# Kernel optimization log

Measured on AMD Instinct MI355X. Metric: run time of the kernel, lower is better.

## Reference

```python
import jax, jax.numpy as jnp
import numpy as np

B = 256
INPUT_DIM = 78464
PC_DIM = 1936
K = 9          # number of step1 sub-models
C = 600        # features per sub-model


def setup_inputs() -> dict:
    key = jax.random.key(0)
    ks = jax.random.split(key, 8)
    x = jax.random.normal(ks[0], (B, INPUT_DIM + 2), dtype=jnp.float32)
    center = jax.random.normal(ks[1], (INPUT_DIM,), dtype=jnp.float32)
    rotation = jax.random.normal(ks[2], (INPUT_DIM, PC_DIM), dtype=jnp.float32) * 0.01
    feats = jax.random.randint(ks[3], (K, C), 0, PC_DIM + 2, dtype=jnp.int32)
    w1 = jax.random.normal(ks[4], (K, C), dtype=jnp.float32) * 0.05   # stacked Linear(C,1) weights
    b1 = jax.random.normal(ks[5], (K,), dtype=jnp.float32)            # stacked biases
    w2 = jax.random.normal(ks[6], (K + 2,), dtype=jnp.float32) * 0.1  # step2 weight
    b2 = jax.random.normal(ks[7], (1,), dtype=jnp.float32)            # step2 bias
    return dict(x=x, center=center, rotation=rotation, feats=feats,
                w1=w1, b1=b1, w2=w2, b2=b2)


def reference(x, center, rotation, feats, w1, b1, w2, b2):
    age = x[:, -1]      # [B]
    female = x[:, -2]   # [B]
    # PCA projection: center and rotate
    p = (x[:, :-2] - center) @ rotation                    # [B, PC_DIM]
    p = jnp.concatenate([p, female[:, None], age[:, None]], axis=1)  # [B, PC_DIM+2]
    # Fused gather + batched tiny GEMMs: 9 Linear(C,1) layers in one einsum
    g = p[:, feats]                                        # [B, K, C]
    s = jnp.einsum('bkc,kc->bk', g, w1) + b1               # [B, K]
    feat2 = jnp.concatenate([s, age[:, None], female[:, None]], axis=1)  # [B, K+2]
    return feat2 @ w2[:, None] + b2                        # [B, 1]
```

## Files before the change

kernel.cpp:

```cpp
#include <hip/hip_runtime.h>

#define IDIM   78464
#define XCOLS  78466
#define PCD    1936
#define PCD2   1938
#define KK     9
#define CC     600
#define BB     256
#define CH     8
#define CHLEN  (IDIM / CH / 2)

typedef float f4 __attribute__((ext_vector_type(4)));
typedef float f2 __attribute__((ext_vector_type(2)));

#define WS_V    0
#define WS_P    2048
#define WS_U    8192

__global__ __launch_bounds__(1024) void k1_buildv(const int* __restrict__ feats,
                                                  const float* __restrict__ w1,
                                                  const float* __restrict__ w2,
                                                  float* __restrict__ v) {
    __shared__ float vl[PCD2];
    for (int i = threadIdx.x; i < PCD2; i += 1024) vl[i] = 0.0f;
    __syncthreads();
    for (int t = threadIdx.x; t < KK * CC; t += 1024) {
        int k = t / CC;
        atomicAdd(&vl[feats[t]], w2[k] * w1[t]);
    }
    __syncthreads();
    for (int i = threadIdx.x; i < PCD2; i += 1024) v[i] = vl[i];
}

__global__ __launch_bounds__(256) void k2_matvec(const float* __restrict__ rot,
                                                 const float* __restrict__ v_in,
                                                 float* __restrict__ u) {
    __shared__ __align__(16) float vlds[PCD];
    for (int i = threadIdx.x; i < PCD; i += 256) vlds[i] = v_in[i];
    __syncthreads();

    const int wave = threadIdx.x >> 6;
    const int lane = threadIdx.x & 63;
    const int nw   = gridDim.x << 2;
    const f4* v4 = reinterpret_cast<const f4*>(vlds);

    for (int row = (blockIdx.x << 2) + wave; row < IDIM; row += nw) {
        const f4* r4 = reinterpret_cast<const f4*>(rot + (size_t)row * PCD);
        float ax = 0.f, ay = 0.f, az = 0.f, aw = 0.f;
        #pragma unroll
        for (int it = 0; it < 7; ++it) {
            int j = lane + (it << 6);
            f4 a = __builtin_nontemporal_load(&r4[j]);
            f4 b = v4[j];
            ax += a.x * b.x; ay += a.y * b.y; az += a.z * b.z; aw += a.w * b.w;
        }
        {
            int j = lane + 448;
            if (j < PCD / 4) {
                f4 a = __builtin_nontemporal_load(&r4[j]);
                f4 b = v4[j];
                ax += a.x * b.x; ay += a.y * b.y; az += a.z * b.z; aw += a.w * b.w;
            }
        }
        float s = (ax + ay) + (az + aw);
        #pragma unroll
        for (int off = 32; off; off >>= 1) s += __shfl_down(s, off, 64);
        if (lane == 0) u[row] = s;
    }
}

__global__ __launch_bounds__(256) void k3_partial(const float* __restrict__ x,
                                                  const float* __restrict__ center,
                                                  const float* __restrict__ u,
                                                  float* __restrict__ part) {
    __shared__ float wred[4];
    const int bid = blockIdx.x;
    const int b = bid >> 3;
    const int c = bid & (CH - 1);
    const float* row = (b < BB) ? (x + (size_t)b * XCOLS) : center;
    const f2* r2 = reinterpret_cast<const f2*>(row);
    const f2* u2 = reinterpret_cast<const f2*>(u);
    const int j0 = c * CHLEN;
    float ax = 0.f, ay = 0.f;
    for (int j = j0 + threadIdx.x; j < j0 + CHLEN; j += 256) {
        f2 a = __builtin_nontemporal_load(&r2[j]);
        f2 uu = u2[j];
        ax += a.x * uu.x; ay += a.y * uu.y;
    }
    float s = ax + ay;
    #pragma unroll
    for (int off = 32; off; off >>= 1) s += __shfl_down(s, off, 64);
    const int wave = threadIdx.x >> 6;
    const int lane = threadIdx.x & 63;
    if (lane == 0) wred[wave] = s;
    __syncthreads();
    if (threadIdx.x == 0) part[bid] = (wred[0] + wred[1]) + (wred[2] + wred[3]);
}

__global__ __launch_bounds__(256) void k4_final(const float* __restrict__ x,
                                                const float* __restrict__ b1,
                                                const float* __restrict__ w2,
                                                const float* __restrict__ b2,
                                                const float* __restrict__ ws,
                                                float* __restrict__ out) {
    int b = threadIdx.x;
    if (b < BB) {
        float female = x[(size_t)b * XCOLS + IDIM];
        float age    = x[(size_t)b * XCOLS + IDIM + 1];
        float s = 0.f, cu = 0.f;
        #pragma unroll
        for (int c = 0; c < CH; ++c) {
            s  += ws[WS_P + b * CH + c];
            cu += ws[WS_P + BB * CH + c];
        }
        float cst = b2[0];
        #pragma unroll
        for (int k = 0; k < KK; ++k) cst += b1[k] * w2[k];
        out[b] = s - cu
               + female * (ws[WS_V + 1936] + w2[10])
               + age    * (ws[WS_V + 1937] + w2[9])
               + cst;
    }
}

extern "C" void kernel_launch(void* const* d_in, const int* in_sizes, int n_in,
                              void* d_out, int out_size, void* d_ws, size_t ws_size,
                              hipStream_t stream) {
    const float* x      = (const float*)d_in[0];
    const float* center = (const float*)d_in[1];
    const float* rot    = (const float*)d_in[2];
    const int*   feats  = (const int*)  d_in[3];
    const float* w1     = (const float*)d_in[4];
    const float* b1     = (const float*)d_in[5];
    const float* w2     = (const float*)d_in[6];
    const float* b2     = (const float*)d_in[7];
    float* ws  = (float*)d_ws;
    float* out = (float*)d_out;

    hipLaunchKernelGGL(k1_buildv,  dim3(1),        dim3(1024), 0, stream, feats, w1, w2, ws + WS_V);
    hipLaunchKernelGGL(k2_matvec,  dim3(2048),     dim3(256),  0, stream, rot, ws + WS_V, ws + WS_U);
    hipLaunchKernelGGL(k3_partial, dim3(257 * CH), dim3(256),  0, stream, x, center, ws + WS_U, ws + WS_P);
    hipLaunchKernelGGL(k4_final,   dim3(1),        dim3(256),  0, stream, x, b1, w2, b2, ws, out);
}
```

Before: 137.0 us.

## Fuse v-build into matvec and final reduction into rowdot via last-block atomic

Result: slower. 184.6 us (+34.8%).

```diff
diff --git a/kernel.cpp b/kernel.cpp
--- a/kernel.cpp
+++ b/kernel.cpp
@@ -9,71 +9,77 @@
 #define BB     256
 #define CH     8
 #define CHLEN  (IDIM / CH / 2)
+#define NBLK_A 2048
+#define NBLK_B ((BB + 1) * CH)
 
 typedef float f4 __attribute__((ext_vector_type(4)));
 typedef float f2 __attribute__((ext_vector_type(2)));
 
-#define WS_V    0
-#define WS_P    2048
+#define WS_V2   0
+#define WS_CNT  2
+#define WS_P    64
 #define WS_U    8192
 
-__global__ __launch_bounds__(1024) void k1_buildv(const int* __restrict__ feats,
-                                                  const float* __restrict__ w1,
-                                                  const float* __restrict__ w2,
-                                                  float* __restrict__ v) {
-    __shared__ float vl[PCD2];
-    for (int i = threadIdx.x; i < PCD2; i += 1024) vl[i] = 0.0f;
+__global__ __launch_bounds__(256) void kA_matvec(const float* __restrict__ rot,
+                                                 const int* __restrict__ feats,
+                                                 const float* __restrict__ w1,
+                                                 const float* __restrict__ w2,
+                                                 float* __restrict__ u,
+                                                 float* __restrict__ ws) {
+    __shared__ __align__(16) float vl[2048];
+    for (int i = threadIdx.x; i < 2048; i += 256) vl[i] = 0.0f;
     __syncthreads();
-    for (int t = threadIdx.x; t < KK * CC; t += 1024) {
+    for (int t = threadIdx.x; t < KK * CC; t += 256) {
         int k = t / CC;
         atomicAdd(&vl[feats[t]], w2[k] * w1[t]);
     }
     __syncthreads();
-    for (int i = threadIdx.x; i < PCD2; i += 1024) v[i] = vl[i];
-}
 
-__global__ __launch_bounds__(256) void k2_matvec(const float* __restrict__ rot,
-                                                 const float* __restrict__ v_in,
-                                                 float* __restrict__ u) {
-    __shared__ __align__(16) float vlds[PCD];
-    for (int i = threadIdx.x; i < PCD; i += 256) vlds[i] = v_in[i];
-    __syncthreads();
+    if (blockIdx.x == 0) {
+        if (threadIdx.x < 2) ws[WS_V2 + threadIdx.x] = vl[PCD + threadIdx.x];
+        if (threadIdx.x == 0) ((int*)ws)[WS_CNT] = 0;
+    }
 
     const int wave = threadIdx.x >> 6;
     const int lane = threadIdx.x & 63;
-    const int nw   = gridDim.x << 2;
-    const f4* v4 = reinterpret_cast<const f4*>(vlds);
+    const f4* v4 = reinterpret_cast<const f4*>(vl);
 
-    for (int row = (blockIdx.x << 2) + wave; row < IDIM; row += nw) {
+    f4 vr0 = v4[lane      ], vr1 = v4[lane +  64], vr2 = v4[lane + 128], vr3 = v4[lane + 192];
+    f4 vr4 = v4[lane + 256], vr5 = v4[lane + 320], vr6 = v4[lane + 384], vr7 = v4[lane + 448];
+    const bool tl = (lane + 448) < (PCD / 4);
+
+    for (int row = (blockIdx.x << 2) + wave; row < IDIM; row += (NBLK_A << 2)) {
         const f4* r4 = reinterpret_cast<const f4*>(rot + (size_t)row * PCD);
-        float ax = 0.f, ay = 0.f, az = 0.f, aw = 0.f;
-        #pragma unroll
-        for (int it = 0; it < 7; ++it) {
-            int j = lane + (it << 6);
-            f4 a = __builtin_nontemporal_load(&r4[j]);
-            f4 b = v4[j];
-            ax += a.x * b.x; ay += a.y * b.y; az += a.z * b.z; aw += a.w * b.w;
-        }
-        {
-            int j = lane + 448;
-            if (j < PCD / 4) {
-                f4 a = __builtin_nontemporal_load(&r4[j]);
-                f4 b = v4[j];
-                ax += a.x * b.x; ay += a.y * b.y; az += a.z * b.z; aw += a.w * b.w;
-            }
-        }
-        float s = (ax + ay) + (az + aw);
+        f4 a0 = __builtin_nontemporal_load(&r4[lane      ]);
+        f4 a1 = __builtin_nontemporal_load(&r4[lane +  64]);
+        f4 a2 = __builtin_nontemporal_load(&r4[lane + 128]);
+        f4 a3 = __builtin_nontemporal_load(&r4[lane + 192]);
+        f4 a4 = __builtin_nontemporal_load(&r4[lane + 256]);
+        f4 a5 = __builtin_nontemporal_load(&r4[lane + 320]);
+        f4 a6 = __builtin_nontemporal_load(&r4[lane + 384]);
+        f4 a7 = (f4)(0.0f);
+        if (tl) a7 = __builtin_nontemporal_load(&r4[lane + 448]);
+
+        f4 acc = a0 * vr0;
+        acc += a1 * vr1;  acc += a2 * vr2;  acc += a3 * vr3;
+        acc += a4 * vr4;  acc += a5 * vr5;  acc += a6 * vr6;  acc += a7 * vr7;
+        float s = (acc.x + acc.y) + (acc.z + acc.w);
         #pragma unroll
         for (int off = 32; off; off >>= 1) s += __shfl_down(s, off, 64);
         if (lane == 0) u[row] = s;
     }
 }
 
-__global__ __launch_bounds__(256) void k3_partial(const float* __restrict__ x,
-                                                  const float* __restrict__ center,
-                                                  const float* __restrict__ u,
-                                                  float* __restrict__ part) {
+__global__ __launch_bounds__(256) void kB_rowdot(const float* __restrict__ x,
+                                                 const float* __restrict__ center,
+                                                 const float* __restrict__ u,
+                                                 const float* __restrict__ b1,
+                                                 const float* __restrict__ w2,
+                                                 const float* __restrict__ b2,
+                                                 float* __restrict__ ws,
+                                                 float* __restrict__ out) {
     __shared__ float wred[4];
+    __shared__ int last;
     const int bid = blockIdx.x;
     const int b = bid >> 3;
     const int c = bid & (CH - 1);
@@ -83,7 +89,7 @@
     const int j0 = c * CHLEN;
     float ax = 0.f, ay = 0.f;
     for (int j = j0 + threadIdx.x; j < j0 + CHLEN; j += 256) {
-        f2 a = __builtin_nontemporal_load(&r2[j]);
+        f2 a  = __builtin_nontemporal_load(&r2[j]);
         f2 uu = u2[j];
         ax += a.x * uu.x; ay += a.y * uu.y;
     }
@@ -94,32 +100,33 @@
     const int lane = threadIdx.x & 63;
     if (lane == 0) wred[wave] = s;
     __syncthreads();
-    if (threadIdx.x == 0) part[bid] = (wred[0] + wred[1]) + (wred[2] + wred[3]);
-}
-
-__global__ __launch_bounds__(256) void k4_final(const float* __restrict__ x,
-                                                const float* __restrict__ b1,
-                                                const float* __restrict__ w2,
-                                                const float* __restrict__ b2,
-                                                const float* __restrict__ ws,
-                                                float* __restrict__ out) {
-    int b = threadIdx.x;
-    if (b < BB) {
-        float female = x[(size_t)b * XCOLS + IDIM];
-        float age    = x[(size_t)b * XCOLS + IDIM + 1];
-        float s = 0.f, cu = 0.f;
-        #pragma unroll
-        for (int c = 0; c < CH; ++c) {
-            s  += ws[WS_P + b * CH + c];
-            cu += ws[WS_P + BB * CH + c];
+    if (threadIdx.x == 0) {
+        ws[WS_P + bid] = (wred[0] + wred[1]) + (wred[2] + wred[3]);
+        __threadfence();
+        int old = atomicAdd((int*)ws + WS_CNT, 1);
+        last = (old == NBLK_B - 1) ? 1 : 0;
+    }
+    __syncthreads();
+    if (last) {
+        __threadfence();
+        int t = threadIdx.x;
+        if (t < BB) {
+            float sm = 0.f, cu = 0.f;
+            #pragma unroll
+            for (int cc = 0; cc < CH; ++cc) {
+                sm += ws[WS_P + t * CH + cc];
+                cu += ws[WS_P + BB * CH + cc];
+            }
+            float female = x[(size_t)t * XCOLS + IDIM];
+            float age    = x[(size_t)t * XCOLS + IDIM + 1];
+            float cst = b2[0];
+            #pragma unroll
+            for (int k = 0; k < KK; ++k) cst += b1[k] * w2[k];
+            out[t] = sm - cu
+                   + female * (ws[WS_V2 + 0] + w2[10])
+                   + age    * (ws[WS_V2 + 1] + w2[9])
+                   + cst;
         }
-        float cst = b2[0];
-        #pragma unroll
-        for (int k = 0; k < KK; ++k) cst += b1[k] * w2[k];
-        out[b] = s - cu
-               + female * (ws[WS_V + 1936] + w2[10])
-               + age    * (ws[WS_V + 1937] + w2[9])
-               + cst;
     }
 }
 
@@ -137,8 +144,8 @@
     float* ws  = (float*)d_ws;
     float* out = (float*)d_out;
 
-    hipLaunchKernelGGL(k1_buildv,  dim3(1),        dim3(1024), 0, stream, feats, w1, w2, ws + WS_V);
-    hipLaunchKernelGGL(k2_matvec,  dim3(2048),     dim3(256),  0, stream, rot, ws + WS_V, ws + WS_U);
-    hipLaunchKernelGGL(k3_partial, dim3(257 * CH), dim3(256),  0, stream, x, center, ws + WS_U, ws + WS_P);
-    hipLaunchKernelGGL(k4_final,   dim3(1),        dim3(256),  0, stream, x, b1, w2, b2, ws, out);
+    hipLaunchKernelGGL(kA_matvec, dim3(NBLK_A), dim3(256), 0, stream,
+                       rot, feats, w1, w2, ws + WS_U, ws);
+    hipLaunchKernelGGL(kB_rowdot, dim3(NBLK_B), dim3(256), 0, stream,
+                       x, center, ws + WS_U, b1, w2, b2, ws, out);
 }
```

## Restructure rotation matvec to block-per-row-range with register-held vector

Applied to the files above, without the earlier changes.

Result: faster. 127.7 us, median of 2 (-6.8%).

```diff
diff --git a/kernel.cpp b/kernel.cpp
--- a/kernel.cpp
+++ b/kernel.cpp
@@ -9,6 +9,10 @@
 #define BB     256
 #define CH     8
 #define CHLEN  (IDIM / CH / 2)
+#define NBLK_B ((BB + 1) * CH)
+
+#define NBLK_A   2048
+#define NBLK_HI  640
 
 typedef float f4 __attribute__((ext_vector_type(4)));
 typedef float f2 __attribute__((ext_vector_type(2)));
@@ -20,7 +24,7 @@
 __global__ __launch_bounds__(1024) void k1_buildv(const int* __restrict__ feats,
                                                   const float* __restrict__ w1,
                                                   const float* __restrict__ w2,
-                                                  float* __restrict__ v) {
+                                                  float* __restrict__ ws) {
     __shared__ float vl[PCD2];
     for (int i = threadIdx.x; i < PCD2; i += 1024) vl[i] = 0.0f;
     __syncthreads();
@@ -29,44 +33,43 @@
         atomicAdd(&vl[feats[t]], w2[k] * w1[t]);
     }
     __syncthreads();
-    for (int i = threadIdx.x; i < PCD2; i += 1024) v[i] = vl[i];
+    for (int i = threadIdx.x; i < PCD2; i += 1024) ws[WS_V + i] = vl[i];
 }
 
 __global__ __launch_bounds__(256) void k2_matvec(const float* __restrict__ rot,
                                                  const float* __restrict__ v_in,
                                                  float* __restrict__ u) {
-    __shared__ __align__(16) float vlds[PCD];
-    for (int i = threadIdx.x; i < PCD; i += 256) vlds[i] = v_in[i];
-    __syncthreads();
+    __shared__ float part[40 * 4];
+    const int tid  = threadIdx.x;
+    const int wave = tid >> 6;
+    const int lane = tid & 63;
+    const int b    = blockIdx.x;
+    const int hi   = (b < NBLK_HI);
+    const int row0 = hi ? b * 39 : NBLK_HI * 39 + (b - NBLK_HI) * 38;
+    const int nrows = hi ? 39 : 38;
 
-    const int wave = threadIdx.x >> 6;
-    const int lane = threadIdx.x & 63;
-    const int nw   = gridDim.x << 2;
-    const f4* v4 = reinterpret_cast<const f4*>(vlds);
+    const f4* v4 = reinterpret_cast<const f4*>(v_in);
+    f4 vr0 = v4[tid];
+    f4 vr1 = (tid < 228) ? v4[256 + tid] : (f4)(0.0f);
 
-    for (int row = (blockIdx.x << 2) + wave; row < IDIM; row += nw) {
-        const f4* r4 = reinterpret_cast<const f4*>(rot + (size_t)row * PCD);
-        float ax = 0.f, ay = 0.f, az = 0.f, aw = 0.f;
-        #pragma unroll
-        for (int it = 0; it < 7; ++it) {
-            int j = lane + (it << 6);
-            f4 a = __builtin_nontemporal_load(&r4[j]);
-            f4 b = v4[j];
-            ax += a.x * b.x; ay += a.y * b.y; az += a.z * b.z; aw += a.w * b.w;
+    const f4* r4 = reinterpret_cast<const f4*>(rot + (size_t)row0 * PCD);
+    for (int r = 0; r < nrows; ++r) {
+        f4 a0 = __builtin_nontemporal_load(&r4[tid]);
+        f4 acc = a0 * vr0;
+        if (tid < 228) {
+            f4 a1 = __builtin_nontemporal_load(&r4[256 + tid]);
+            acc += a1 * vr1;
         }
-        {
-            int j = lane + 448;
-            if (j < PCD / 4) {
-                f4 a = __builtin_nontemporal_load(&r4[j]);
-                f4 b = v4[j];
-                ax += a.x * b.x; ay += a.y * b.y; az += a.z * b.z; aw += a.w * b.w;
-            }
-        }
-        float s = (ax + ay) + (az + aw);
+        float s = (acc.x + acc.y) + (acc.z + acc.w);
         #pragma unroll
         for (int off = 32; off; off >>= 1) s += __shfl_down(s, off, 64);
-        if (lane == 0) u[row] = s;
+        if (lane == 0) part[r * 4 + wave] = s;
+        r4 += PCD / 4;
     }
+    __syncthreads();
+    if (tid < nrows)
+        u[row0 + tid] = (part[tid * 4 + 0] + part[tid * 4 + 1])
+                      + (part[tid * 4 + 2] + part[tid * 4 + 3]);
 }
 
 __global__ __launch_bounds__(256) void k3_partial(const float* __restrict__ x,
@@ -83,7 +86,7 @@
     const int j0 = c * CHLEN;
     float ax = 0.f, ay = 0.f;
     for (int j = j0 + threadIdx.x; j < j0 + CHLEN; j += 256) {
-        f2 a = __builtin_nontemporal_load(&r2[j]);
+        f2 a  = __builtin_nontemporal_load(&r2[j]);
         f2 uu = u2[j];
         ax += a.x * uu.x; ay += a.y * uu.y;
     }
@@ -137,8 +140,8 @@
     float* ws  = (float*)d_ws;
     float* out = (float*)d_out;
 
-    hipLaunchKernelGGL(k1_buildv,  dim3(1),        dim3(1024), 0, stream, feats, w1, w2, ws + WS_V);
-    hipLaunchKernelGGL(k2_matvec,  dim3(2048),     dim3(256),  0, stream, rot, ws + WS_V, ws + WS_U);
-    hipLaunchKernelGGL(k3_partial, dim3(257 * CH), dim3(256),  0, stream, x, center, ws + WS_U, ws + WS_P);
-    hipLaunchKernelGGL(k4_final,   dim3(1),        dim3(256),  0, stream, x, b1, w2, b2, ws, out);
+    hipLaunchKernelGGL(k1_buildv, dim3(1),      dim3(1024), 0, stream, feats, w1, w2, ws);
+    hipLaunchKernelGGL(k2_matvec, dim3(NBLK_A), dim3(256),  0, stream, rot, ws + WS_V, ws + WS_U);
+    hipLaunchKernelGGL(k3_partial, dim3(NBLK_B), dim3(256), 0, stream, x, center, ws + WS_U, ws + WS_P);
+    hipLaunchKernelGGL(k4_final,  dim3(1),      dim3(256),  0, stream, x, b1, w2, b2, ws, out);
 }
```
